# Kernel tuning notes

Measured on AMD Instinct MI355X. Metric: run time of the kernel, lower is better.

## Reference

```python
import jax, jax.numpy as jnp
import numpy as np
from itertools import combinations

# ---- G(3,0,1) projective geometric algebra tables (blade order: grades 0..4, lexicographic) ----

def _build_tables():
    blades = [c for g in range(5) for c in combinations(range(4), g)]
    index = {b: i for i, b in enumerate(blades)}
    def mul(a, b, e0_sq):
        lst = list(a) + list(b)
        sign = 1
        for i in range(len(lst)):
            for j in range(len(lst) - 1 - i):
                if lst[j] > lst[j + 1]:
                    lst[j], lst[j + 1] = lst[j + 1], lst[j]
                    sign = -sign
        out, i = [], 0
        while i < len(lst):
            if i + 1 < len(lst) and lst[i] == lst[i + 1]:
                if lst[i] == 0:
                    sign *= e0_sq  # e0^2 = 0 in PGA geometric product
                i += 2
            else:
                out.append(lst[i]); i += 1
        return tuple(out), sign
    GP = np.zeros((16, 16, 16), np.float32)
    WEDGE = np.zeros((16, 16, 16), np.float32)
    for a in blades:
        for b in blades:
            bl, s = mul(a, b, 0)
            if s != 0:
                GP[index[a], index[b], index[bl]] += s
            if not (set(a) & set(b)):
                bl, s = mul(a, b, 1)
                WEDGE[index[a], index[b], index[bl]] += s
    D = np.zeros((16, 16), np.float32)
    for a in blades:
        c = tuple(sorted(set(range(4)) - set(a)))
        bl, s = mul(a, c, 1)  # e_a ^ e_c = s * e0123
        D[index[c], index[a]] = s
    Dinv = np.linalg.inv(D).astype(np.float32)
    # 9 Pin(3,0,1)-equivariant linear basis maps: 5 grade projections + 4 left-mult by e0
    B = np.zeros((9, 16, 16), np.float32)
    for i, a in enumerate(blades):
        B[len(a), i, i] = 1.0
        if 0 not in a:
            tgt = tuple(sorted((0,) + a))
            B[5 + len(a), index[tgt], i] = 1.0
    inner_idx = np.array([i for i, a in enumerate(blades) if 0 not in a])  # invariant inner product skips e0 blades
    return (jnp.asarray(GP), jnp.asarray(WEDGE), jnp.asarray(D), jnp.asarray(Dinv), jnp.asarray(B), jnp.asarray(inner_idx))

GP_T, WEDGE_T, DUAL, DUAL_INV, BASIS, INNER_IDX = _build_tables()
N_HEADS = 8  # gatr SelfAttentionConfig default


def equi_linear(x, W):
    # x: [..., in_ch, 16], W: [out_ch, in_ch, 9] -> [..., out_ch, 16]
    return jnp.einsum('...ik,oib,bjk->...oj', x, W, BASIS)


def equi_norm(x, eps=1e-6):
    sq = jnp.sum(jnp.take(x, INNER_IDX, axis=-1) ** 2, axis=-1)      # [..., C]
    factor = jnp.mean(sq, axis=-1, keepdims=True)[..., None]          # [..., 1, 1]
    return x * jax.lax.rsqrt(factor + eps)


def geometric_product(x, y):
    return jnp.einsum('...i,...j,ijk->...k', x, y, GP_T)


def equi_join(x, y):
    xd = jnp.einsum('ji,...i->...j', DUAL, x)
    yd = jnp.einsum('ji,...i->...j', DUAL, y)
    w = jnp.einsum('...i,...j,ijk->...k', xd, yd, WEDGE_T)
    return jnp.einsum('ji,...i->...j', DUAL_INV, w)


def attention(x, Wq, Wk, Wv, Wo):
    Bb, N, C, _ = x.shape
    ch = C // N_HEADS
    def split(h):
        return h.reshape(Bb, N, N_HEADS, ch, 16).transpose(0, 2, 1, 3, 4)  # [B,H,N,ch,16]
    q = split(equi_linear(x, Wq))
    k = split(equi_linear(x, Wk))
    v = split(equi_linear(x, Wv))
    qi = jnp.take(q, INNER_IDX, axis=-1)
    ki = jnp.take(k, INNER_IDX, axis=-1)
    logits = jnp.einsum('bhnck,bhmck->bhnm', qi, ki) / np.float32(np.sqrt(8 * ch))
    att = jax.nn.softmax(logits, axis=-1)
    out = jnp.einsum('bhnm,bhmck->bhnck', att, v)
    out = out.transpose(0, 2, 1, 3, 4).reshape(Bb, N, C, 16)
    return equi_linear(out, Wo)


def geo_mlp(x, Wl, Wr, Wm):
    C = x.shape[-2]
    half = C // 2
    left = equi_linear(x, Wl)
    right = equi_linear(x, Wr)
    gp = geometric_product(left[..., :half, :], right[..., :half, :])
    jn = equi_join(left[..., half:, :], right[..., half:, :])
    h = jnp.concatenate([gp, jn], axis=-2)
    h = h * jax.nn.gelu(h[..., 0:1], approximate=False)  # scalar-gated GELU
    return equi_linear(h, Wm)


def embed_point(p):
    # PGA point: homogeneous trivector, e123 coefficient 1
    z = jnp.zeros(p.shape[:-1] + (16,), p.dtype)
    z = z.at[..., 11].set(p[..., 2])
    z = z.at[..., 12].set(-p[..., 1])
    z = z.at[..., 13].set(p[..., 0])
    z = z.at[..., 14].set(1.0)
    return z


def reference(points, W_in, Wq, Wk, Wv, Wo, Wl, Wr, Wm, W_out):
    x = embed_point(points)[..., None, :]   # [B, N, 1, 16]
    x = equi_linear(x, W_in)                # [B, N, C, 16]
    def block(xc, p):
        wq, wk, wv, wo, wl, wr, wm = p
        xc = xc + attention(equi_norm(xc), wq, wk, wv, wo)
        xc = xc + geo_mlp(equi_norm(xc), wl, wr, wm)
        return xc, None
    x, _ = jax.lax.scan(block, x, (Wq, Wk, Wv, Wo, Wl, Wr, Wm))
    out = equi_linear(x, W_out)             # [B, N, 1, 16]
    return jnp.mean(out[..., 0], axis=(1, 2))  # [B]


def setup_inputs():
    key = jax.random.key(0)
    ks = jax.random.split(key, 12)
    B, N, C, L = 1, 2048, 16, 10
    def w(k, o, i):
        return jax.random.normal(k, (o, i, 9), jnp.float32) / np.float32(np.sqrt(9.0 * i))
    def wl(k, o, i):
        return jax.random.normal(k, (L, o, i, 9), jnp.float32) / np.float32(np.sqrt(9.0 * i))
    return {
        'points': jax.random.normal(ks[0], (B, N, 3), jnp.float32),
        'W_in': w(ks[1], C, 1),
        'Wq': wl(ks[2], C, C), 'Wk': wl(ks[3], C, C), 'Wv': wl(ks[4], C, C),
        'Wo': wl(ks[5], C, C), 'Wl': wl(ks[6], C, C), 'Wr': wl(ks[7], C, C),
        'Wm': wl(ks[8], C, C), 'W_out': w(ks[9], 1, C),
    }
```

## Files before the change

kernel.cpp:

```cpp
#include <hip/hip_runtime.h>
#include <hip/hip_bf16.h>
#include <math.h>

#define NTOK 2048

typedef short short8v __attribute__((ext_vector_type(8)));
typedef short short4v __attribute__((ext_vector_type(4)));
typedef float f32x4 __attribute__((ext_vector_type(4)));
typedef unsigned u32x4 __attribute__((ext_vector_type(4)));

__device__ __forceinline__ unsigned short f2bf(float x){
  unsigned u = __float_as_uint(x);
  u += 0x7fff + ((u>>16)&1);
  return (unsigned short)(u>>16);
}
__device__ __forceinline__ unsigned pack_bf2(float a, float b){
  __hip_bfloat162 h = __float22bfloat162_rn(float2{a,b});
  return *reinterpret_cast<unsigned*>(&h);
}

struct GEnt { unsigned char i, j, k; signed char s; };

constexpr int IDX2MASK[16] = {0,1,2,4,8,3,5,9,6,10,12,7,11,13,14,15};
constexpr int MASK2IDX[16] = {0,1,2,5,3,6,8,11,4,7,9,12,10,13,14,15};

constexpr int rsign(int a, int b){
  int cnt=0;
  for(int i=0;i<4;++i) if((b>>i)&1) for(int j=i+1;j<4;++j) if((a>>j)&1) cnt++;
  return (cnt&1)?-1:1;
}

struct GPTab { GEnt e[192]; };
constexpr GPTab make_gp(){
  GPTab t{}; int n=0;
  for(int ia=0; ia<16; ++ia) for(int ib=0; ib<16; ++ib){
    int a=IDX2MASK[ia], b=IDX2MASK[ib];
    if(a&b&1) continue;
    t.e[n].i=(unsigned char)ia; t.e[n].j=(unsigned char)ib;
    t.e[n].k=(unsigned char)MASK2IDX[a^b]; t.e[n].s=(signed char)rsign(a,b);
    ++n;
  }
  return t;
}
static constexpr GPTab GP_TAB = make_gp();

struct JTab { GEnt e[81]; };
constexpr JTab make_join(){
  JTab t{}; int n=0;
  for(int ia=0; ia<16; ++ia) for(int ib=0; ib<16; ++ib){
    int a=IDX2MASK[ia], b=IDX2MASK[ib];
    if((a|b)!=15) continue;
    int ca=(~a)&15, cb=(~b)&15, k=a&b, ck=(~k)&15;
    int s = rsign(a,ca)*rsign(b,cb)*rsign(ca,cb)*rsign(k,ck);
    t.e[n].i=(unsigned char)ia; t.e[n].j=(unsigned char)ib;
    t.e[n].k=(unsigned char)MASK2IDX[k]; t.e[n].s=(signed char)s;
    ++n;
  }
  return t;
}
static constexpr JTab J_TAB = make_join();

constexpr int INNER[8] = {0,2,3,4,8,9,10,14};

__device__ __forceinline__ void apply_gp(float* o, const float* a, const float* b){
#pragma unroll
  for(int n=0;n<192;++n){
    const float s = (float)GP_TAB.e[n].s;
    o[GP_TAB.e[n].k] = fmaf(s*a[GP_TAB.e[n].i], b[GP_TAB.e[n].j], o[GP_TAB.e[n].k]);
  }
}
__device__ __forceinline__ void apply_join(float* o, const float* a, const float* b){
#pragma unroll
  for(int n=0;n<81;++n){
    const float s = (float)J_TAB.e[n].s;
    o[J_TAB.e[n].k] = fmaf(s*a[J_TAB.e[n].i], b[J_TAB.e[n].j], o[J_TAB.e[n].k]);
  }
}

__device__ __forceinline__ void elin_row(float acc[16], const float* xin, const float* w0p){
#pragma unroll
  for(int j=0;j<16;++j) acc[j]=0.0f;
#pragma unroll
  for(int i=0;i<16;++i){
    const float* w = w0p + i*9;
    const float4* xp = (const float4*)(xin + i*16);
    float4 A=xp[0], B=xp[1], Cc=xp[2], D=xp[3];
    float w0=w[0],w1=w[1],w2=w[2],w3=w[3],w4=w[4],w5=w[5],w6=w[6],w7=w[7],w8=w[8];
    acc[0] = fmaf(w0, A.x,  acc[0]);
    acc[1] = fmaf(w1, A.y,  acc[1]);
    acc[2] = fmaf(w1, A.z,  acc[2]);
    acc[3] = fmaf(w1, A.w,  acc[3]);
    acc[4] = fmaf(w1, B.x,  acc[4]);
    acc[5] = fmaf(w2, B.y,  acc[5]);
    acc[6] = fmaf(w2, B.z,  acc[6]);
    acc[7] = fmaf(w2, B.w,  acc[7]);
    acc[8] = fmaf(w2, Cc.x, acc[8]);
    acc[9] = fmaf(w2, Cc.y, acc[9]);
    acc[10]= fmaf(w2, Cc.z, acc[10]);
    acc[11]= fmaf(w3, Cc.w, acc[11]);
    acc[12]= fmaf(w3, D.x,  acc[12]);
    acc[13]= fmaf(w3, D.y,  acc[13]);
    acc[14]= fmaf(w3, D.z,  acc[14]);
    acc[15]= fmaf(w4, D.w,  acc[15]);
    acc[1] = fmaf(w5, A.x,  acc[1]);
    acc[5] = fmaf(w6, A.z,  acc[5]);
    acc[6] = fmaf(w6, A.w,  acc[6]);
    acc[7] = fmaf(w6, B.x,  acc[7]);
    acc[11]= fmaf(w7, Cc.x, acc[11]);
    acc[12]= fmaf(w7, Cc.y, acc[12]);
    acc[13]= fmaf(w7, Cc.z, acc[13]);
    acc[15]= fmaf(w8, D.z,  acc[15]);
  }
}

__device__ __forceinline__ float gelu_exact(float x){
  return 0.5f*x*(1.0f+erff(x*0.70710678118654752f));
}

#define WPAD 145
#define TBS  264
#define TPB  8

template<int MODE>
__global__ __launch_bounds__(128) void token_kernel(
    const float* __restrict__ points, const float* __restrict__ Win,
    const float* __restrict__ Wo, const float* __restrict__ Wl,
    const float* __restrict__ Wr, const float* __restrict__ Wm,
    const float* __restrict__ Wq, const float* __restrict__ Wk,
    const float* __restrict__ Wv, const float* __restrict__ Wout,
    const float* __restrict__ ATT, float* __restrict__ X,
    unsigned short* __restrict__ Qg16, unsigned short* __restrict__ Kg16,
    unsigned short* __restrict__ VgT, float* __restrict__ toksum)
{
  __shared__ float wlds[6*16*WPAD];
  __shared__ float buf[TPB*TBS];
  __shared__ float sred[TPB*16];
  const int tid = threadIdx.x;
  const int t = tid>>4, o = tid&15;
  const int n = blockIdx.x*TPB + t;

  auto stage = [&](float* dst, const float* src){
#pragma unroll
    for(int r=0;r<18;++r){
      int k = tid + r*128;
      dst[(k/144)*WPAD + (k%144)] = src[k];
    }
  };
  if (MODE==0){ stage(wlds+3*16*WPAD, Wq); stage(wlds+4*16*WPAD, Wk); stage(wlds+5*16*WPAD, Wv); }
  if (MODE==1){ stage(wlds+0*16*WPAD, Wl); stage(wlds+1*16*WPAD, Wr); stage(wlds+2*16*WPAD, Wm);
                stage(wlds+3*16*WPAD, Wq); stage(wlds+4*16*WPAD, Wk); stage(wlds+5*16*WPAD, Wv); }
  if (MODE==2){ stage(wlds+0*16*WPAD, Wl); stage(wlds+1*16*WPAD, Wr); stage(wlds+2*16*WPAD, Wm); }

  float* tb = buf + t*TBS;
  float xr[16];

  if (MODE==0){
    float px = points[n*3+0], py = points[n*3+1], pz = points[n*3+2];
    float w3 = Win[o*9+3], w8 = Win[o*9+8];
#pragma unroll
    for(int j=0;j<16;++j) xr[j]=0.0f;
    xr[11]= w3*pz; xr[12]= -w3*py; xr[13]= w3*px; xr[14]= w3; xr[15]= w8;
    float4* xg = (float4*)(X + (size_t)n*256 + o*16);
    xg[0]=make_float4(xr[0],xr[1],xr[2],xr[3]);
    xg[1]=make_float4(xr[4],xr[5],xr[6],xr[7]);
    xg[2]=make_float4(xr[8],xr[9],xr[10],xr[11]);
    xg[3]=make_float4(xr[12],xr[13],xr[14],xr[15]);
  } else {
    const float4* xg = (const float4*)(X + (size_t)n*256 + o*16);
    float4 a=xg[0],b=xg[1],c=xg[2],d=xg[3];
    xr[0]=a.x; xr[1]=a.y; xr[2]=a.z; xr[3]=a.w;
    xr[4]=b.x; xr[5]=b.y; xr[6]=b.z; xr[7]=b.w;
    xr[8]=c.x; xr[9]=c.y; xr[10]=c.z; xr[11]=c.w;
    xr[12]=d.x; xr[13]=d.y; xr[14]=d.z; xr[15]=d.w;
    const float4* ag = (const float4*)(ATT + (size_t)n*256 + o*16);
    float4* bp = (float4*)(tb + o*16);
    bp[0]=ag[0]; bp[1]=ag[1]; bp[2]=ag[2]; bp[3]=ag[3];
    __syncthreads();
    float acc[16];
    elin_row(acc, tb, Wo + o*144);
#pragma unroll
    for(int j=0;j<16;++j) xr[j]+=acc[j];
    float s=0;
#pragma unroll
    for(int z=0;z<8;++z){ float v=xr[INNER[z]]; s=fmaf(v,v,s); }
    sred[tid]=s; __syncthreads();
    float tot=0;
#pragma unroll
    for(int c2=0;c2<16;++c2) tot += sred[t*16+c2];
    float f = 1.0f/sqrtf(tot*(1.0f/16.0f)+1e-6f);
    float4* bp2=(float4*)(tb+o*16);
    bp2[0]=make_float4(xr[0]*f,xr[1]*f,xr[2]*f,xr[3]*f);
    bp2[1]=make_float4(xr[4]*f,xr[5]*f,xr[6]*f,xr[7]*f);
    bp2[2]=make_float4(xr[8]*f,xr[9]*f,xr[10]*f,xr[11]*f);
    bp2[3]=make_float4(xr[12]*f,xr[13]*f,xr[14]*f,xr[15]*f);
    __syncthreads();
    float L[16], R[16];
    elin_row(L, tb, wlds+0*16*WPAD + o*WPAD);
    elin_row(R, tb, wlds+1*16*WPAD + o*WPAD);
    float h[16];
#pragma unroll
    for(int j=0;j<16;++j) h[j]=0.0f;
    if (o<8) apply_gp(h,L,R); else apply_join(h,L,R);
    float gel = gelu_exact(h[0]);
#pragma unroll
    for(int j=0;j<16;++j) h[j]*=gel;
    __syncthreads();
    float4* bp3=(float4*)(tb+o*16);
    bp3[0]=make_float4(h[0],h[1],h[2],h[3]);
    bp3[1]=make_float4(h[4],h[5],h[6],h[7]);
    bp3[2]=make_float4(h[8],h[9],h[10],h[11]);
    bp3[3]=make_float4(h[12],h[13],h[14],h[15]);
    __syncthreads();
    float mm2[16];
    elin_row(mm2, tb, wlds+2*16*WPAD + o*WPAD);
#pragma unroll
    for(int j=0;j<16;++j) xr[j]+=mm2[j];
    if (MODE==1){
      float4* xs = (float4*)(X + (size_t)n*256 + o*16);
      xs[0]=make_float4(xr[0],xr[1],xr[2],xr[3]);
      xs[1]=make_float4(xr[4],xr[5],xr[6],xr[7]);
      xs[2]=make_float4(xr[8],xr[9],xr[10],xr[11]);
      xs[3]=make_float4(xr[12],xr[13],xr[14],xr[15]);
    }
  }

  if (MODE==2){
    sred[tid] = Wout[o*9]*xr[0];
    __syncthreads();
    if (o==0){
      float s2=0;
#pragma unroll
      for(int c2=0;c2<16;++c2) s2+=sred[t*16+c2];
      toksum[n]=s2;
    }
    return;
  }

  {
    float s=0;
#pragma unroll
    for(int z=0;z<8;++z){ float v=xr[INNER[z]]; s=fmaf(v,v,s); }
    sred[tid]=s; __syncthreads();
    float tot=0;
#pragma unroll
    for(int c2=0;c2<16;++c2) tot += sred[t*16+c2];
    float f2 = 1.0f/sqrtf(tot*(1.0f/16.0f)+1e-6f);
    float4* bp4=(float4*)(tb+o*16);
    bp4[0]=make_float4(xr[0]*f2,xr[1]*f2,xr[2]*f2,xr[3]*f2);
    bp4[1]=make_float4(xr[4]*f2,xr[5]*f2,xr[6]*f2,xr[7]*f2);
    bp4[2]=make_float4(xr[8]*f2,xr[9]*f2,xr[10]*f2,xr[11]*f2);
    bp4[3]=make_float4(xr[12]*f2,xr[13]*f2,xr[14]*f2,xr[15]*f2);
    __syncthreads();
    float q_[16],k_[16],v_[16];
    elin_row(q_, tb, wlds+3*16*WPAD+o*WPAD);
    elin_row(k_, tb, wlds+4*16*WPAD+o*WPAD);
    elin_row(v_, tb, wlds+5*16*WPAD+o*WPAD);
    int hh=o>>1, cc=o&1;
    {
      unsigned qw[4], kw[4];
#pragma unroll
      for(int j=0;j<4;++j){
        unsigned short a0=f2bf(q_[INNER[2*j]]*0.25f), a1=f2bf(q_[INNER[2*j+1]]*0.25f);
        unsigned short b0=f2bf(k_[INNER[2*j]]),       b1=f2bf(k_[INNER[2*j+1]]);
        qw[j] = (unsigned)a0 | ((unsigned)a1<<16);
        kw[j] = (unsigned)b0 | ((unsigned)b1<<16);
      }
      size_t rb = ((size_t)hh*NTOK + n)*16 + cc*8;
      *(uint4*)(Qg16 + rb) = make_uint4(qw[0],qw[1],qw[2],qw[3]);
      *(uint4*)(Kg16 + rb) = make_uint4(kw[0],kw[1],kw[2],kw[3]);
    }
    __syncthreads();
    {
      float4* vb = (float4*)(tb + o*16);
      vb[0]=make_float4(v_[0],v_[1],v_[2],v_[3]);
      vb[1]=make_float4(v_[4],v_[5],v_[6],v_[7]);
      vb[2]=make_float4(v_[8],v_[9],v_[10],v_[11]);
      vb[3]=make_float4(v_[12],v_[13],v_[14],v_[15]);
    }
    __syncthreads();
#pragma unroll
    for(int pp=0;pp<2;++pp){
      int p  = tid + pp*128;
      int h2 = p>>5, v2 = p&31;
      int oc = 2*h2 + (v2>>4), c2 = v2&15;
      unsigned vw[4];
#pragma unroll
      for(int j=0;j<4;++j){
        unsigned short e0=f2bf(buf[(2*j  )*TBS + oc*16 + c2]);
        unsigned short e1=f2bf(buf[(2*j+1)*TBS + oc*16 + c2]);
        vw[j]=(unsigned)e0 | ((unsigned)e1<<16);
      }
      *(uint4*)(VgT + ((size_t)(h2*32+v2))*NTOK + (size_t)blockIdx.x*TPB) = make_uint4(vw[0],vw[1],vw[2],vw[3]);
    }
  }
}

__global__ __launch_bounds__(256) void attn_kernel(
    const unsigned short* __restrict__ Qg16, const unsigned short* __restrict__ Kg16,
    const unsigned short* __restrict__ VgT,  float* __restrict__ ATT)
{
  __shared__ float cmb[4*32*17];
  __shared__ float ml[4*16*2];
  const int tid = threadIdx.x;
  const int l   = tid & 63, w = tid >> 6;
  const int h   = blockIdx.x >> 7, qb = blockIdx.x & 127;
  const int l15 = l & 15, lg = l >> 4;

  const short4v z4 = {0,0,0,0};
  short8v qf;
  {
    const short4v* qp = (const short4v*)(Qg16 + ((size_t)(h*NTOK + qb*16 + l15))*16 + lg*4);
    qf = __builtin_shufflevector(*qp, z4, 0,1,2,3,4,5,6,7);
  }

  f32x4 acc0 = {0,0,0,0}, acc1 = {0,0,0,0};
  float m = -INFINITY, ls = 0.0f;
  const int key0 = w*512;
  const size_t vrow = ((size_t)(h*32 + l15))*NTOK;

#pragma unroll 2
  for(int kc=0; kc<512; kc+=64){
    f32x4 S[4];
#pragma unroll
    for(int t2=0;t2<4;++t2){
      const short4v* kp = (const short4v*)(Kg16 + ((size_t)(h*NTOK + key0 + kc + t2*16 + l15))*16 + lg*4);
      short8v kf = __builtin_shufflevector(*kp, z4, 0,1,2,3,4,5,6,7);
      f32x4 z = {0,0,0,0};
      S[t2] = __builtin_amdgcn_mfma_f32_16x16x32_bf16(kf, qf, z, 0,0,0);
    }
    float mx = S[0][0];
#pragma unroll
    for(int t2=0;t2<4;++t2)
#pragma unroll
      for(int r=0;r<4;++r) mx = fmaxf(mx, S[t2][r]);
    mx = fmaxf(mx, __shfl_xor(mx, 16));
    mx = fmaxf(mx, __shfl_xor(mx, 32));
    float nm = fmaxf(m, mx);
    float corr = __expf(m - nm);
    m = nm;
    float p[4][4];
    float s = 0.0f;
#pragma unroll
    for(int t2=0;t2<4;++t2)
#pragma unroll
      for(int r=0;r<4;++r){ float pv = __expf(S[t2][r]-nm); p[t2][r]=pv; s += pv; }
    s += __shfl_xor(s, 16);
    s += __shfl_xor(s, 32);
    ls = ls*corr + s;
    float c0 = __shfl(corr, lg*4+0);
    float c1 = __shfl(corr, lg*4+1);
    float c2 = __shfl(corr, lg*4+2);
    float c3 = __shfl(corr, lg*4+3);
    acc0[0]*=c0; acc0[1]*=c1; acc0[2]*=c2; acc0[3]*=c3;
    acc1[0]*=c0; acc1[1]*=c1; acc1[2]*=c2; acc1[3]*=c3;
    u32x4 paw, paw2;
    paw[0]=pack_bf2(p[0][0],p[0][1]); paw[1]=pack_bf2(p[0][2],p[0][3]);
    paw[2]=pack_bf2(p[1][0],p[1][1]); paw[3]=pack_bf2(p[1][2],p[1][3]);
    paw2[0]=pack_bf2(p[2][0],p[2][1]); paw2[1]=pack_bf2(p[2][2],p[2][3]);
    paw2[2]=pack_bf2(p[3][0],p[3][1]); paw2[3]=pack_bf2(p[3][2],p[3][3]);
    short8v pa  = *reinterpret_cast<short8v*>(&paw);
    short8v pa2 = *reinterpret_cast<short8v*>(&paw2);
    size_t vb = vrow + key0 + kc;
    const short4v* v0a = (const short4v*)(VgT + vb + lg*4);
    const short4v* v0b = (const short4v*)(VgT + vb + 16 + lg*4);
    const short4v* v0c = (const short4v*)(VgT + vb + 32 + lg*4);
    const short4v* v0d = (const short4v*)(VgT + vb + 48 + lg*4);
    short8v vb0  = __builtin_shufflevector(*v0a, *v0b, 0,1,2,3,4,5,6,7);
    short8v vb0b = __builtin_shufflevector(*v0c, *v0d, 0,1,2,3,4,5,6,7);
    size_t vb1s = vb + (size_t)16*NTOK;
    const short4v* v1a = (const short4v*)(VgT + vb1s + lg*4);
    const short4v* v1b = (const short4v*)(VgT + vb1s + 16 + lg*4);
    const short4v* v1c = (const short4v*)(VgT + vb1s + 32 + lg*4);
    const short4v* v1d = (const short4v*)(VgT + vb1s + 48 + lg*4);
    short8v vb1  = __builtin_shufflevector(*v1a, *v1b, 0,1,2,3,4,5,6,7);
    short8v vb1b = __builtin_shufflevector(*v1c, *v1d, 0,1,2,3,4,5,6,7);
    acc0 = __builtin_amdgcn_mfma_f32_16x16x32_bf16(pa,  vb0,  acc0, 0,0,0);
    acc0 = __builtin_amdgcn_mfma_f32_16x16x32_bf16(pa2, vb0b, acc0, 0,0,0);
    acc1 = __builtin_amdgcn_mfma_f32_16x16x32_bf16(pa,  vb1,  acc1, 0,0,0);
    acc1 = __builtin_amdgcn_mfma_f32_16x16x32_bf16(pa2, vb1b, acc1, 0,0,0);
  }

  {
    float* cw = cmb + w*544;
#pragma unroll
    for(int r=0;r<4;++r){
      cw[ l15     *17 + lg*4 + r] = acc0[r];
      cw[(l15+16) *17 + lg*4 + r] = acc1[r];
    }
    if (lg == 0){
      ml[(w*16 + l15)*2]   = m;
      ml[(w*16 + l15)*2+1] = ls;
    }
  }
  __syncthreads();
  {
    int q = tid & 15, v = tid >> 4;
    float M = -INFINITY;
#pragma unroll
    for(int w2=0; w2<4; ++w2) M = fmaxf(M, ml[(w2*16+q)*2]);
    float L=0, a0=0, a1=0;
#pragma unroll
    for(int w2=0; w2<4; ++w2){
      float ww = __expf(ml[(w2*16+q)*2] - M);
      L  = fmaf(ml[(w2*16+q)*2+1], ww, L);
      a0 = fmaf(cmb[w2*544 +  v     *17 + q], ww, a0);
      a1 = fmaf(cmb[w2*544 + (v+16) *17 + q], ww, a1);
    }
    float inv = 1.0f/L;
    int n = qb*16 + q;
    ATT[(size_t)n*256 + (size_t)(2*h  )*16 + v] = a0*inv;
    ATT[(size_t)n*256 + (size_t)(2*h+1)*16 + v] = a1*inv;
  }
}

__global__ __launch_bounds__(256) void reduce_kernel(const float* __restrict__ tok, float* __restrict__ out){
  int tid=threadIdx.x;
  float s=0;
  for(int i=tid;i<NTOK;i+=256) s+=tok[i];
#pragma unroll
  for(int off=32;off>0;off>>=1) s += __shfl_down(s,off);
  __shared__ float red[4];
  if((tid&63)==0) red[tid>>6]=s;
  __syncthreads();
  if(tid==0) out[0]=(red[0]+red[1]+red[2]+red[3])*(1.0f/2048.0f);
}

extern "C" void kernel_launch(void* const* d_in, const int* in_sizes, int n_in,
                              void* d_out, int out_size, void* d_ws, size_t ws_size,
                              hipStream_t stream){
  const float* points=(const float*)d_in[0];
  const float* Win=(const float*)d_in[1];
  const float* Wq=(const float*)d_in[2];
  const float* Wk=(const float*)d_in[3];
  const float* Wv=(const float*)d_in[4];
  const float* Wo=(const float*)d_in[5];
  const float* Wl=(const float*)d_in[6];
  const float* Wr=(const float*)d_in[7];
  const float* Wm=(const float*)d_in[8];
  const float* Wout=(const float*)d_in[9];
  float* ws=(float*)d_ws;
  float* X    = ws;
  float* ATT  = ws + 524288;
  unsigned short* Qg16 = (unsigned short*)(ws + 1048576);
  unsigned short* Kg16 = (unsigned short*)(ws + 1179648);
  unsigned short* VgT  = (unsigned short*)(ws + 1310720);
  float* tok  = ws + 1572864;
  float* out=(float*)d_out;

  token_kernel<0><<<256,128,0,stream>>>(points,Win,nullptr,nullptr,nullptr,nullptr,
                                        Wq,Wk,Wv,nullptr,nullptr,X,Qg16,Kg16,VgT,nullptr);
  for(int l=0;l<10;++l){
    attn_kernel<<<1024,256,0,stream>>>(Qg16,Kg16,VgT,ATT);
    if(l<9){
      token_kernel<1><<<256,128,0,stream>>>(nullptr,nullptr,
          Wo+l*2304,Wl+l*2304,Wr+l*2304,Wm+l*2304,
          Wq+(l+1)*2304,Wk+(l+1)*2304,Wv+(l+1)*2304,nullptr,
          ATT,X,Qg16,Kg16,VgT,nullptr);
    } else {
      token_kernel<2><<<256,128,0,stream>>>(nullptr,nullptr,
          Wo+l*2304,Wl+l*2304,Wr+l*2304,Wm+l*2304,
          nullptr,nullptr,nullptr,Wout,
          ATT,X,nullptr,nullptr,nullptr,tok);
    }
  }
  reduce_kernel<<<1,256,0,stream>>>(tok,out);
}
```

Measured before the change: 664.4 us.

## Use two-pass softmax with precomputed row max in attention kernel

```diff
diff --git a/kernel.cpp b/kernel.cpp
--- a/kernel.cpp
+++ b/kernel.cpp
@@ -313,11 +313,27 @@
     qf = __builtin_shufflevector(*qp, z4, 0,1,2,3,4,5,6,7);
   }
 
-  f32x4 acc0 = {0,0,0,0}, acc1 = {0,0,0,0};
-  float m = -INFINITY, ls = 0.0f;
   const int key0 = w*512;
   const size_t vrow = ((size_t)(h*32 + l15))*NTOK;
 
+  float mx = -INFINITY;
+#pragma unroll 2
+  for(int kc=0; kc<512; kc+=64){
+#pragma unroll
+    for(int t2=0;t2<4;++t2){
+      const short4v* kp = (const short4v*)(Kg16 + ((size_t)(h*NTOK + key0 + kc + t2*16 + l15))*16 + lg*4);
+      short8v kf = __builtin_shufflevector(*kp, z4, 0,1,2,3,4,5,6,7);
+      f32x4 z = {0,0,0,0};
+      f32x4 S = __builtin_amdgcn_mfma_f32_16x16x32_bf16(kf, qf, z, 0,0,0);
+      mx = fmaxf(mx, fmaxf(fmaxf(S[0],S[1]), fmaxf(S[2],S[3])));
+    }
+  }
+  mx = fmaxf(mx, __shfl_xor(mx, 16));
+  mx = fmaxf(mx, __shfl_xor(mx, 32));
+  const float M = mx;
+
+  f32x4 acc0 = {0,0,0,0}, acc1 = {0,0,0,0};
+  float ls = 0.0f;
 #pragma unroll 2
   for(int kc=0; kc<512; kc+=64){
     f32x4 S[4];
@@ -328,31 +344,11 @@
       f32x4 z = {0,0,0,0};
       S[t2] = __builtin_amdgcn_mfma_f32_16x16x32_bf16(kf, qf, z, 0,0,0);
     }
-    float mx = S[0][0];
+    float p[4][4];
 #pragma unroll
     for(int t2=0;t2<4;++t2)
 #pragma unroll
-      for(int r=0;r<4;++r) mx = fmaxf(mx, S[t2][r]);
-    mx = fmaxf(mx, __shfl_xor(mx, 16));
-    mx = fmaxf(mx, __shfl_xor(mx, 32));
-    float nm = fmaxf(m, mx);
-    float corr = __expf(m - nm);
-    m = nm;
-    float p[4][4];
-    float s = 0.0f;
-#pragma unroll
-    for(int t2=0;t2<4;++t2)
-#pragma unroll
-      for(int r=0;r<4;++r){ float pv = __expf(S[t2][r]-nm); p[t2][r]=pv; s += pv; }
-    s += __shfl_xor(s, 16);
-    s += __shfl_xor(s, 32);
-    ls = ls*corr + s;
-    float c0 = __shfl(corr, lg*4+0);
-    float c1 = __shfl(corr, lg*4+1);
-    float c2 = __shfl(corr, lg*4+2);
-    float c3 = __shfl(corr, lg*4+3);
-    acc0[0]*=c0; acc0[1]*=c1; acc0[2]*=c2; acc0[3]*=c3;
-    acc1[0]*=c0; acc1[1]*=c1; acc1[2]*=c2; acc1[3]*=c3;
+      for(int r=0;r<4;++r){ float pv = __expf(S[t2][r]-M); p[t2][r]=pv; ls += pv; }
     u32x4 paw, paw2;
     paw[0]=pack_bf2(p[0][0],p[0][1]); paw[1]=pack_bf2(p[0][2],p[0][3]);
     paw[2]=pack_bf2(p[1][0],p[1][1]); paw[3]=pack_bf2(p[1][2],p[1][3]);
@@ -379,6 +375,8 @@
     acc1 = __builtin_amdgcn_mfma_f32_16x16x32_bf16(pa,  vb1,  acc1, 0,0,0);
     acc1 = __builtin_amdgcn_mfma_f32_16x16x32_bf16(pa2, vb1b, acc1, 0,0,0);
   }
+  ls += __shfl_xor(ls, 16);
+  ls += __shfl_xor(ls, 32);
 
   {
     float* cw = cmb + w*544;
@@ -388,20 +386,20 @@
       cw[(l15+16) *17 + lg*4 + r] = acc1[r];
     }
     if (lg == 0){
-      ml[(w*16 + l15)*2]   = m;
+      ml[(w*16 + l15)*2]   = M;
       ml[(w*16 + l15)*2+1] = ls;
     }
   }
   __syncthreads();
   {
     int q = tid & 15, v = tid >> 4;
-    float M = -INFINITY;
-#pragma unroll
-    for(int w2=0; w2<4; ++w2) M = fmaxf(M, ml[(w2*16+q)*2]);
+    float Mg = -INFINITY;
+#pragma unroll
+    for(int w2=0; w2<4; ++w2) Mg = fmaxf(Mg, ml[(w2*16+q)*2]);
     float L=0, a0=0, a1=0;
 #pragma unroll
     for(int w2=0; w2<4; ++w2){
-      float ww = __expf(ml[(w2*16+q)*2] - M);
+      float ww = __expf(ml[(w2*16+q)*2] - Mg);
       L  = fmaf(ml[(w2*16+q)*2+1], ww, L);
       a0 = fmaf(cmb[w2*544 +  v     *17 + q], ww, a0);
       a1 = fmaf(cmb[w2*544 + (v+16) *17 + q], ww, a1);
```

Result: slower. 692.6 us (+4.2%).
